# Optimization experiments

Hardware: AMD Instinct MI355X
Metric: run time of the kernel (lower is better)

The kernel has to match this reference:

```python
import jax, jax.numpy as jnp
import numpy as np

B, N, C = 8, 4096, 768
H = 12
D = C // H  # 64


def setup_inputs() -> dict:
    key = jax.random.key(0)
    k1, k2, k3 = jax.random.split(key, 3)
    x = jax.random.normal(k1, (B, N, C), dtype=jnp.float32)
    Wqkv = jax.random.normal(k2, (C, 3 * C), dtype=jnp.float32) * (C ** -0.5)
    Wproj = jax.random.normal(k3, (C, C), dtype=jnp.float32) * (C ** -0.5)
    bproj = jnp.zeros((C,), dtype=jnp.float32)
    return {"x": x, "Wqkv": Wqkv, "Wproj": Wproj, "bproj": bproj}


def reference(x, Wqkv, Wproj, bproj):
    b, n, c = x.shape
    qkv = x @ Wqkv  # [B,N,3C]
    qkv = qkv.reshape(b, n, 3, H, D).transpose(2, 0, 3, 1, 4)  # [3,B,H,N,D]
    q, k, v = qkv[0], qkv[1], qkv[2]
    # softmax over the sequence axis (dim=-2 in torch => N)
    k = jax.nn.softmax(k, axis=-2)
    # context: [B,H,D,D] -- small d x d intermediate
    context = jnp.einsum('bhnd,bhne->bhde', k, v)
    out = jnp.einsum('bhnd,bhde->bhne', q, context)  # [B,H,N,D]
    out = out.transpose(0, 2, 1, 3).reshape(b, n, c)  # b h n d -> b n (h d)
    return out @ Wproj + bproj
```

## Files before the change

kernel.cpp:

```cpp
#include <hip/hip_runtime.h>
#include <cstdint>
#include <cstddef>


typedef __bf16 bf8_t __attribute__((ext_vector_type(8)));
typedef float f4_t __attribute__((ext_vector_type(4)));

#define DEV_INLINE __device__ __forceinline__

DEV_INLINE void gload16(const void* g, void* l) {
  __builtin_amdgcn_global_load_lds(
      (const __attribute__((address_space(1))) void*)g,
      (__attribute__((address_space(3))) void*)l, 16, 0, 0);
}

__global__ __launch_bounds__(256) void cast_f32_bf16(const float* __restrict__ in,
                                                     __bf16* __restrict__ out, int n4) {
  int i = blockIdx.x * 256 + threadIdx.x;
  if (i >= n4) return;
  float4 f = ((const float4*)in)[i];
  union { __bf16 h[4]; uint2 u; } o;
  o.h[0] = (__bf16)f.x; o.h[1] = (__bf16)f.y; o.h[2] = (__bf16)f.z; o.h[3] = (__bf16)f.w;
  ((uint2*)out)[i] = o.u;
}

__global__ __launch_bounds__(256) void transpose_cast(const float* __restrict__ in,
                                                      __bf16* __restrict__ out, int R, int C) {
  __shared__ float t[64][65];
  const int tilesR = R >> 6;
  const int tr = blockIdx.x % tilesR, tc = blockIdx.x / tilesR;
  const int tx = threadIdx.x & 63, ty = threadIdx.x >> 6;
  const int r0 = tr * 64, c0 = tc * 64;
#pragma unroll
  for (int p = 0; p < 16; p++) {
    int r = p * 4 + ty;
    t[r][tx] = in[(size_t)(r0 + r) * C + c0 + tx];
  }
  __syncthreads();
#pragma unroll
  for (int p = 0; p < 16; p++) {
    int c = p * 4 + ty;
    out[(size_t)(c0 + c) * R + r0 + tx] = (__bf16)t[tx][c];
  }
}

__global__ __launch_bounds__(256) void wq_cast(const float* __restrict__ in,
                                               __bf16* __restrict__ out) {
  int o = blockIdx.x * 256 + threadIdx.x;
  int r = o / 768, c = o - r * 768;
  out[o] = (__bf16)in[r * 2304 + c];
}


#define SA_(buf, u, kc) gload16(gA + (size_t)((u) * 64) * 768 + (kc), dAl + (buf) * 16384 + (u) * 4096)
#define SB_(buf, u, kc) gload16(gB + (size_t)((u) * 64) * 768 + (kc), dBl + (buf) * 8192 + (u) * 4096)

#define PH_(q, STAGE, TAIL) do {                                              \
    bf8_t af[2][2], bfr[2][2];                                                \
    _Pragma("unroll") for (int i_ = 0; i_ < 2; i_++)                          \
      _Pragma("unroll") for (int ks_ = 0; ks_ < 2; ks_++) {                   \
        af[i_][ks_]  = *(const bf8_t*)(aB + offA[2 * ((q) >> 1) + i_][ks_]);  \
        bfr[i_][ks_] = *(const bf8_t*)(bB + offB[2 * ((q) & 1) + i_][ks_]);   \
      }                                                                       \
    STAGE;                                                                    \
    __builtin_amdgcn_s_barrier();                                             \
    __builtin_amdgcn_s_setprio(1);                                            \
    _Pragma("unroll") for (int ks_ = 0; ks_ < 2; ks_++)                       \
      _Pragma("unroll") for (int i_ = 0; i_ < 2; i_++)                        \
        _Pragma("unroll") for (int j_ = 0; j_ < 2; j_++)                      \
          acc[2 * ((q) >> 1) + i_][2 * ((q) & 1) + j_] =                      \
            __builtin_amdgcn_mfma_f32_16x16x32_bf16(af[i_][ks_], bfr[j_][ks_],\
              acc[2 * ((q) >> 1) + i_][2 * ((q) & 1) + j_], 0, 0, 0);         \
    __builtin_amdgcn_s_setprio(0);                                            \
    TAIL;                                                                     \
    __builtin_amdgcn_s_barrier();                                             \
  } while (0)

#define MAIN_LOOP() do {                                                      \
    SA_(0, 0, 0); SA_(0, 1, 0); SA_(0, 2, 0); SA_(0, 3, 0);                   \
    SB_(0, 0, 0); SB_(0, 1, 0);                                               \
    SA_(1, 0, 64); SA_(1, 1, 64); SA_(1, 2, 64); SA_(1, 3, 64);               \
    SB_(1, 0, 64); SB_(1, 1, 64);                                             \
    asm volatile("s_waitcnt vmcnt(6)" ::: "memory");                          \
    __builtin_amdgcn_s_barrier();                                             \
    int cur = 0;                                                              \
    for (int t = 0; t < 10; t++) {                                            \
      const __bf16* aB = sA + cur * 16384;                                    \
      const __bf16* bB = sB + cur * 8192;                                     \
      int nx = cur + 2; if (nx > 2) nx -= 3;                                  \
      const int kc = (t + 2) * 64;                                            \
      PH_(0, { SA_(nx, 0, kc); SA_(nx, 1, kc); }, {});                        \
      PH_(1, { SA_(nx, 2, kc); SA_(nx, 3, kc); }, {});                        \
      PH_(2, { SB_(nx, 0, kc); }, {});                                        \
      PH_(3, { SB_(nx, 1, kc); },                                             \
          { asm volatile("s_waitcnt vmcnt(6)" ::: "memory"); });              \
      cur++; if (cur > 2) cur = 0;                                            \
    }                                                                         \
    { const __bf16* aB = sA + cur * 16384;                                    \
      const __bf16* bB = sB + cur * 8192;                                     \
      PH_(0, {}, {}); PH_(1, {}, {}); PH_(2, {}, {});                         \
      PH_(3, {}, { asm volatile("s_waitcnt vmcnt(0)" ::: "memory"); });       \
      cur++; if (cur > 2) cur = 0; }                                          \
    { const __bf16* aB = sA + cur * 16384;                                    \
      const __bf16* bB = sB + cur * 8192;                                     \
      PH_(0, {}, {}); PH_(1, {}, {}); PH_(2, {}, {}); PH_(3, {}, {}); }       \
  } while (0)

#define GEMM_SETUP()                                                          \
  const int tid = threadIdx.x;                                                \
  const int trow = tid >> 3;                                                  \
  const int gcol = ((tid & 7) ^ (trow & 7)) * 8;                              \
  __bf16* dAl = sA + tid * 8;                                                 \
  __bf16* dBl = sB + tid * 8;                                                 \
  const int lane = tid & 63, wv = tid >> 6;                                   \
  const int wm = wv >> 1, wn = wv & 1;                                        \
  const int lr = lane & 15, quad = lane >> 4, rsw = lr & 7;                   \
  int offA[4][2], offB[4][2];                                                 \
  _Pragma("unroll") for (int f_ = 0; f_ < 4; f_++)                            \
    _Pragma("unroll") for (int ks_ = 0; ks_ < 2; ks_++) {                     \
      offA[f_][ks_] = (wm * 64 + f_ * 16 + lr) * 64 + (((ks_ * 4 + quad) ^ rsw) * 8); \
      offB[f_][ks_] = (wn * 64 + f_ * 16 + lr) * 64 + (((ks_ * 4 + quad) ^ rsw) * 8); \
    }                                                                         \
  f4_t acc[4][4];                                                             \
  _Pragma("unroll") for (int i_ = 0; i_ < 4; i_++)                            \
    _Pragma("unroll") for (int j_ = 0; j_ < 4; j_++)                          \
      acc[i_][j_] = (f4_t){0.f, 0.f, 0.f, 0.f};

__global__ __launch_bounds__(512, 2) void gemm1_kv(const __bf16* __restrict__ A,
                                                   const __bf16* __restrict__ B,
                                                   __bf16* __restrict__ KTo,
                                                   __bf16* __restrict__ VTo) {
  __shared__ __bf16 sA[3 * 16384];
  __shared__ __bf16 sB[3 * 8192];
  const int xcd = blockIdx.x & 7, g = blockIdx.x >> 3;
  const int mt = xcd * 16 + g / 12, nt = g % 12;
  GEMM_SETUP();
  const __bf16* gA = A + (size_t)(mt * 256 + trow) * 768 + gcol;
  const __bf16* gB = B + (size_t)(nt * 128 + trow) * 768 + gcol;

  MAIN_LOOP();

  const int s = nt / 6;
  __bf16* T = s ? VTo : KTo;
  const int colbase = (nt % 6) * 128 + wn * 64;
  const int bidx = mt >> 4;
  const int nbase = (mt & 15) * 256 + wm * 64 + quad * 4;
#pragma unroll
  for (int ci = 0; ci < 4; ci++) {
    int col = colbase + ci * 16 + lr;
    int h = col >> 6, d = col & 63;
    __bf16* Tp = T + ((size_t)(bidx * 12 + h) * 64 + d) * 4096;
#pragma unroll
    for (int ri = 0; ri < 4; ri++) {
      union { __bf16 h4[4]; uint2 u2; } pk;
#pragma unroll
      for (int r = 0; r < 4; r++) pk.h4[r] = (__bf16)acc[ri][ci][r];
      *(uint2*)&Tp[nbase + ri * 16] = pk.u2;
    }
  }
}

__global__ __launch_bounds__(256) void stats_rows(const __bf16* __restrict__ KT,
                                                  float2* __restrict__ stats) {
  __shared__ float red[8];
  const __bf16* p = KT + (size_t)blockIdx.x * 4096;
  const int tid = threadIdx.x, lane = tid & 63, wv = tid >> 6;
  bf8_t x0 = *(const bf8_t*)&p[tid * 16];
  bf8_t x1 = *(const bf8_t*)&p[tid * 16 + 8];
  float v[16];
#pragma unroll
  for (int k = 0; k < 8; k++) { v[k] = (float)x0[k]; v[8 + k] = (float)x1[k]; }
  float m = v[0];
#pragma unroll
  for (int k = 1; k < 16; k++) m = fmaxf(m, v[k]);
  for (int o = 32; o; o >>= 1) m = fmaxf(m, __shfl_xor(m, o, 64));
  if (lane == 0) red[wv] = m;
  __syncthreads();
  m = fmaxf(fmaxf(red[0], red[1]), fmaxf(red[2], red[3]));
  float s = 0.f;
#pragma unroll
  for (int k = 0; k < 16; k++) s += __expf(v[k] - m);
  for (int o = 32; o; o >>= 1) s += __shfl_xor(s, o, 64);
  if (lane == 0) red[4 + wv] = s;
  __syncthreads();
  if (tid == 0) {
    float st = red[4] + red[5] + red[6] + red[7];
    stats[blockIdx.x] = make_float2(m, 1.0f / st);
  }
}

__global__ __launch_bounds__(256) void ctx_kernel(const __bf16* __restrict__ KT,
                                                  const __bf16* __restrict__ VT,
                                                  const float2* __restrict__ stats,
                                                  float* __restrict__ part) {
  const int bh = blockIdx.x >> 3, kc = blockIdx.x & 7;
  const int tid = threadIdx.x, lane = tid & 63, wv = tid >> 6;
  const int wr = (wv >> 1) * 32, wc = (wv & 1) * 32;
  const int lr = lane & 15, quad = lane >> 4;
  const __bf16* Ab = KT + (size_t)bh * 64 * 4096;
  const __bf16* Bb = VT + (size_t)bh * 64 * 4096;
  float2 st[2];
  st[0] = stats[bh * 64 + wr + lr];
  st[1] = stats[bh * 64 + wr + 16 + lr];
  const f4_t fz = {0.f, 0.f, 0.f, 0.f};
  f4_t acc[2][2] = {{fz, fz}, {fz, fz}};
  const int kbeg = kc * 512;
  for (int k0 = kbeg; k0 < kbeg + 512; k0 += 32) {
    bf8_t a[2], b[2];
#pragma unroll
    for (int i = 0; i < 2; i++) {
      bf8_t raw = *(const bf8_t*)&Ab[(size_t)(wr + i * 16 + lr) * 4096 + k0 + quad * 8];
#pragma unroll
      for (int e = 0; e < 8; e++)
        a[i][e] = (__bf16)(__expf((float)raw[e] - st[i].x) * st[i].y);
    }
#pragma unroll
    for (int j = 0; j < 2; j++)
      b[j] = *(const bf8_t*)&Bb[(size_t)(wc + j * 16 + lr) * 4096 + k0 + quad * 8];
#pragma unroll
    for (int i = 0; i < 2; i++)
#pragma unroll
      for (int j = 0; j < 2; j++)
        acc[i][j] = __builtin_amdgcn_mfma_f32_16x16x32_bf16(a[i], b[j], acc[i][j], 0, 0, 0);
  }
  float* po = part + (size_t)blockIdx.x * 4096;
#pragma unroll
  for (int i = 0; i < 2; i++)
#pragma unroll
    for (int j = 0; j < 2; j++)
#pragma unroll
      for (int r = 0; r < 4; r++)
        po[(wr + i * 16 + quad * 4 + r) * 64 + wc + j * 16 + lr] = acc[i][j][r];
}

__global__ __launch_bounds__(256) void wfused_kernel(const float* __restrict__ part,
                                                     const __bf16* __restrict__ WpT,
                                                     __bf16* __restrict__ B2T) {
  __shared__ __bf16 sctx[64 * 64];
  const int bh = blockIdx.x, cblk = blockIdx.y;
  const int b = bh / 12, h = bh % 12;
  const int tid = threadIdx.x;
  for (int i = tid; i < 4096; i += 256) {
    float s = 0.f;
#pragma unroll
    for (int kc = 0; kc < 8; kc++) s += part[(size_t)(bh * 8 + kc) * 4096 + i];
    sctx[i] = (__bf16)s;
  }
  __syncthreads();
  const int lane = tid & 63, wv = tid >> 6, lr = lane & 15, quad = lane >> 4;
  const int c0 = cblk * 192 + wv * 48;
  const f4_t fz = {0.f, 0.f, 0.f, 0.f};
  f4_t acc[3][4];
#pragma unroll
  for (int i = 0; i < 3; i++)
#pragma unroll
    for (int j = 0; j < 4; j++) acc[i][j] = fz;
#pragma unroll
  for (int k0 = 0; k0 < 64; k0 += 32) {
    bf8_t a[3], bq[4];
#pragma unroll
    for (int i = 0; i < 3; i++)
      a[i] = *(const bf8_t*)&WpT[(size_t)(c0 + i * 16 + lr) * 768 + h * 64 + k0 + quad * 8];
#pragma unroll
    for (int j = 0; j < 4; j++)
      bq[j] = *(const bf8_t*)&sctx[(j * 16 + lr) * 64 + k0 + quad * 8];
#pragma unroll
    for (int i = 0; i < 3; i++)
#pragma unroll
      for (int j = 0; j < 4; j++)
        acc[i][j] = __builtin_amdgcn_mfma_f32_16x16x32_bf16(a[i], bq[j], acc[i][j], 0, 0, 0);
  }
#pragma unroll
  for (int i = 0; i < 3; i++)
#pragma unroll
    for (int j = 0; j < 4; j++)
#pragma unroll
      for (int r = 0; r < 4; r++) {
        int c = c0 + i * 16 + quad * 4 + r;
        int d = j * 16 + lr;
        B2T[((size_t)b * 768 + c) * 768 + h * 64 + d] = (__bf16)acc[i][j][r];
      }
}

__global__ __launch_bounds__(256) void combine_kernel(const __bf16* __restrict__ B2Tall,
                                                      const __bf16* __restrict__ Wq,
                                                      __bf16* __restrict__ Wcomb) {
  constexpr int LD = 768, BK = 32, KTOT = 768;
  __shared__ __bf16 sAc[64 * 32];
  __shared__ __bf16 sBc[64 * 32];
  const int b = blockIdx.x / 144, rem = blockIdx.x % 144;
  const int mt = rem / 12, nt = rem % 12;
  const __bf16* A = B2Tall + (size_t)b * 768 * 768;
  const int tid = threadIdx.x, lane = tid & 63, wv = tid >> 6;
  const int wr = (wv >> 1) * 32, wc = (wv & 1) * 32;
  const int lr = lane & 15, quad = lane >> 4;

  const int e0 = tid * 8;
  const int srow = e0 >> 5, skk = e0 & 31;
  const __bf16* gA = A + (size_t)(mt * 64 + srow) * LD + skk;
  const __bf16* gB = Wq + (size_t)(nt * 64 + srow) * LD + skk;

  const f4_t fz = {0.f, 0.f, 0.f, 0.f};
  f4_t acc[2][2] = {{fz, fz}, {fz, fz}};

  for (int k0 = 0; k0 < KTOT; k0 += BK) {
    gload16(gA, &sAc[e0]);
    gload16(gB, &sBc[e0]);
    gA += BK; gB += BK;
    __syncthreads();
    bf8_t a[2], bq[2];
#pragma unroll
    for (int i = 0; i < 2; i++)
      a[i] = *(const bf8_t*)&sAc[(wr + i * 16 + lr) * 32 + quad * 8];
#pragma unroll
    for (int j = 0; j < 2; j++)
      bq[j] = *(const bf8_t*)&sBc[(wc + j * 16 + lr) * 32 + quad * 8];
#pragma unroll
    for (int i = 0; i < 2; i++)
#pragma unroll
      for (int j = 0; j < 2; j++)
        acc[i][j] = __builtin_amdgcn_mfma_f32_16x16x32_bf16(a[i], bq[j], acc[i][j], 0, 0, 0);
    __syncthreads();
  }
  __bf16* C = Wcomb + (size_t)b * 768 * 768;
  const int row0 = mt * 64 + wr, col0 = nt * 64 + wc;
#pragma unroll
  for (int i = 0; i < 2; i++)
#pragma unroll
    for (int j = 0; j < 2; j++)
#pragma unroll
      for (int r = 0; r < 4; r++)
        C[(size_t)(row0 + i * 16 + quad * 4 + r) * 768 + col0 + j * 16 + lr] =
            (__bf16)acc[i][j][r];
}

__global__ __launch_bounds__(512, 2) void gemm2_out(const __bf16* __restrict__ A,
                                                    const __bf16* __restrict__ Ball,
                                                    float* __restrict__ C,
                                                    const float* __restrict__ bias) {
  __shared__ __bf16 sA[3 * 16384];
  __shared__ __bf16 sB[3 * 8192];
  const int xcd = blockIdx.x & 7, g = blockIdx.x >> 3;
  const int mt = xcd * 16 + g / 6, nt = g % 6;
  const __bf16* B = Ball + (size_t)(mt >> 4) * 768 * 768;
  GEMM_SETUP();
  const __bf16* gA = A + (size_t)(mt * 256 + trow) * 768 + gcol;
  const __bf16* gB = B + (size_t)(nt * 128 + trow) * 768 + gcol;

  MAIN_LOOP();

  const int row0 = mt * 256 + wm * 64 + quad * 4;
  const int col0 = nt * 128 + wn * 64;
#pragma unroll
  for (int ci = 0; ci < 4; ci++) {
    int col = col0 + ci * 16 + lr;
    float bv = bias[col];
#pragma unroll
    for (int ri = 0; ri < 4; ri++) {
#pragma unroll
      for (int r = 0; r < 4; r++)
        C[(size_t)(row0 + ri * 16 + r) * 768 + col] = acc[ri][ci][r] + bv;
    }
  }
}

extern "C" void kernel_launch(void* const* d_in, const int* in_sizes, int n_in,
                              void* d_out, int out_size, void* d_ws, size_t ws_size,
                              hipStream_t stream) {
  const float* x = (const float*)d_in[0];
  const float* Wqkv = (const float*)d_in[1];
  const float* Wproj = (const float*)d_in[2];
  const float* bproj = (const float*)d_in[3];
  float* out = (float*)d_out;

  char* ws = (char*)d_ws;
  __bf16* Xb    = (__bf16*)(ws + 0);
  __bf16* KT    = (__bf16*)(ws + 50331648);
  __bf16* VT    = (__bf16*)(ws + 100663296);
  __bf16* WqkvT = (__bf16*)(ws + 150994944);
  float2* stats = (float2*)(ws + 150994944);
  __bf16* Wqc   = (__bf16*)(ws + 154533888);
  __bf16* WpT   = (__bf16*)(ws + 155713536);
  float*  part  = (float*)(ws + 156893184);
  __bf16* B2T   = (__bf16*)(ws + 169476096);
  __bf16* Wcomb = (__bf16*)(ws + 178913280);

  cast_f32_bf16<<<24576, 256, 0, stream>>>(x, Xb, 25165824 / 4);
  transpose_cast<<<12 * 36, 256, 0, stream>>>(Wqkv, WqkvT, 768, 2304);
  wq_cast<<<(768 * 768) / 256, 256, 0, stream>>>(Wqkv, Wqc);
  transpose_cast<<<12 * 12, 256, 0, stream>>>(Wproj, WpT, 768, 768);
  gemm1_kv<<<1536, 512, 0, stream>>>(Xb, WqkvT + 768 * 768, KT, VT);
  stats_rows<<<6144, 256, 0, stream>>>(KT, stats);
  ctx_kernel<<<96 * 8, 256, 0, stream>>>(KT, VT, stats, part);
  wfused_kernel<<<dim3(96, 4), 256, 0, stream>>>(part, WpT, B2T);
  combine_kernel<<<1152, 256, 0, stream>>>(B2T, Wqc, Wcomb);
  gemm2_out<<<768, 512, 0, stream>>>(Xb, Wcomb, out, bproj);
}
```

Baseline: 438.6 us.

## Enlarge GEMM tiles to 256x256 with BK=32 and 8x4 accumulators per wave

```diff
diff --git a/kernel.cpp b/kernel.cpp
--- a/kernel.cpp
+++ b/kernel.cpp
@@ -52,110 +52,121 @@
 }
 
 
-#define SA_(buf, u, kc) gload16(gA + (size_t)((u) * 64) * 768 + (kc), dAl + (buf) * 16384 + (u) * 4096)
-#define SB_(buf, u, kc) gload16(gB + (size_t)((u) * 64) * 768 + (kc), dBl + (buf) * 8192 + (u) * 4096)
-
-#define PH_(q, STAGE, TAIL) do {                                              \
-    bf8_t af[2][2], bfr[2][2];                                                \
-    _Pragma("unroll") for (int i_ = 0; i_ < 2; i_++)                          \
-      _Pragma("unroll") for (int ks_ = 0; ks_ < 2; ks_++) {                   \
-        af[i_][ks_]  = *(const bf8_t*)(aB + offA[2 * ((q) >> 1) + i_][ks_]);  \
-        bfr[i_][ks_] = *(const bf8_t*)(bB + offB[2 * ((q) & 1) + i_][ks_]);   \
-      }                                                                       \
-    STAGE;                                                                    \
+#define MFMA16(aa, bb, cc) cc = __builtin_amdgcn_mfma_f32_16x16x32_bf16(aa, bb, cc, 0, 0, 0)
+
+#define SAu(buf, u, kc) gload16(gA + (size_t)((u) * 128) * 768 + (kc),        \
+                                sA + (buf) * 8192 + (u) * 4096 + tid * 8)
+#define SBu(buf, u, kc) gload16(gB + (size_t)((u) * 128) * 768 + (kc),        \
+                                sB + (buf) * 8192 + (u) * 4096 + tid * 8)
+#define STAGE_T(buf, kc) do { SAu(buf,0,kc); SAu(buf,1,kc); SBu(buf,0,kc); SBu(buf,1,kc); } while (0)
+
+#define G_SETUP()                                                             \
+  const int tid = threadIdx.x;                                                \
+  const int srow = tid >> 2;                                                  \
+  const int gcol = ((tid & 3) ^ (srow & 3)) * 8;                              \
+  const int lane = tid & 63, wv = tid >> 6;                                   \
+  const int wm = wv >> 2, wn = wv & 3;                                        \
+  const int lr = lane & 15, quad = lane >> 4;                                 \
+  const int ksw = (quad ^ (lr & 3)) * 8;                                      \
+  const int offA0 = (wm * 128 + lr) * 32 + ksw;                               \
+  const int offB0 = (wn * 64 + lr) * 32 + ksw;                                \
+  f4_t acc[8][4];                                                             \
+  _Pragma("unroll") for (int i_ = 0; i_ < 8; i_++)                            \
+    _Pragma("unroll") for (int j_ = 0; j_ < 4; j_++)                          \
+      acc[i_][j_] = (f4_t){0.f, 0.f, 0.f, 0.f};
+
+#define G_ITER(SA_STAGE, SB_STAGE, TAILV) do {                                \
+    const __bf16* aBp = sA + cur * 8192;                                      \
+    const __bf16* bBp = sB + cur * 8192;                                      \
+    bf8_t a0, a1, a2, a3, b0, b1, b2, b3;                                     \
+    a0 = *(const bf8_t*)(aBp + offA0);                                        \
+    a1 = *(const bf8_t*)(aBp + offA0 + 512);                                  \
+    a2 = *(const bf8_t*)(aBp + offA0 + 1024);                                 \
+    a3 = *(const bf8_t*)(aBp + offA0 + 1536);                                 \
+    b0 = *(const bf8_t*)(bBp + offB0);                                        \
+    b1 = *(const bf8_t*)(bBp + offB0 + 512);                                  \
+    b2 = *(const bf8_t*)(bBp + offB0 + 1024);                                 \
+    b3 = *(const bf8_t*)(bBp + offB0 + 1536);                                 \
+    SA_STAGE;                                                                 \
     __builtin_amdgcn_s_barrier();                                             \
     __builtin_amdgcn_s_setprio(1);                                            \
-    _Pragma("unroll") for (int ks_ = 0; ks_ < 2; ks_++)                       \
-      _Pragma("unroll") for (int i_ = 0; i_ < 2; i_++)                        \
-        _Pragma("unroll") for (int j_ = 0; j_ < 2; j_++)                      \
-          acc[2 * ((q) >> 1) + i_][2 * ((q) & 1) + j_] =                      \
-            __builtin_amdgcn_mfma_f32_16x16x32_bf16(af[i_][ks_], bfr[j_][ks_],\
-              acc[2 * ((q) >> 1) + i_][2 * ((q) & 1) + j_], 0, 0, 0);         \
+    MFMA16(a0, b0, acc[0][0]); MFMA16(a0, b1, acc[0][1]);                     \
+    MFMA16(a0, b2, acc[0][2]); MFMA16(a0, b3, acc[0][3]);                     \
+    MFMA16(a1, b0, acc[1][0]); MFMA16(a1, b1, acc[1][1]);                     \
+    MFMA16(a1, b2, acc[1][2]); MFMA16(a1, b3, acc[1][3]);                     \
+    MFMA16(a2, b0, acc[2][0]); MFMA16(a2, b1, acc[2][1]);                     \
+    MFMA16(a2, b2, acc[2][2]); MFMA16(a2, b3, acc[2][3]);                     \
+    MFMA16(a3, b0, acc[3][0]); MFMA16(a3, b1, acc[3][1]);                     \
+    MFMA16(a3, b2, acc[3][2]); MFMA16(a3, b3, acc[3][3]);                     \
     __builtin_amdgcn_s_setprio(0);                                            \
-    TAIL;                                                                     \
+    __builtin_amdgcn_s_barrier();                                             \
+    a0 = *(const bf8_t*)(aBp + offA0 + 2048);                                 \
+    a1 = *(const bf8_t*)(aBp + offA0 + 2560);                                 \
+    a2 = *(const bf8_t*)(aBp + offA0 + 3072);                                 \
+    a3 = *(const bf8_t*)(aBp + offA0 + 3584);                                 \
+    SB_STAGE;                                                                 \
+    __builtin_amdgcn_s_barrier();                                             \
+    __builtin_amdgcn_s_setprio(1);                                            \
+    MFMA16(a0, b0, acc[4][0]); MFMA16(a0, b1, acc[4][1]);                     \
+    MFMA16(a0, b2, acc[4][2]); MFMA16(a0, b3, acc[4][3]);                     \
+    MFMA16(a1, b0, acc[5][0]); MFMA16(a1, b1, acc[5][1]);                     \
+    MFMA16(a1, b2, acc[5][2]); MFMA16(a1, b3, acc[5][3]);                     \
+    MFMA16(a2, b0, acc[6][0]); MFMA16(a2, b1, acc[6][1]);                     \
+    MFMA16(a2, b2, acc[6][2]); MFMA16(a2, b3, acc[6][3]);                     \
+    MFMA16(a3, b0, acc[7][0]); MFMA16(a3, b1, acc[7][1]);                     \
+    MFMA16(a3, b2, acc[7][2]); MFMA16(a3, b3, acc[7][3]);                     \
+    __builtin_amdgcn_s_setprio(0);                                            \
+    TAILV;                                                                    \
     __builtin_amdgcn_s_barrier();                                             \
   } while (0)
 
-#define MAIN_LOOP() do {                                                      \
-    SA_(0, 0, 0); SA_(0, 1, 0); SA_(0, 2, 0); SA_(0, 3, 0);                   \
-    SB_(0, 0, 0); SB_(0, 1, 0);                                               \
-    SA_(1, 0, 64); SA_(1, 1, 64); SA_(1, 2, 64); SA_(1, 3, 64);               \
-    SB_(1, 0, 64); SB_(1, 1, 64);                                             \
-    asm volatile("s_waitcnt vmcnt(6)" ::: "memory");                          \
+#define G_MAIN() do {                                                         \
+    STAGE_T(0, 0); STAGE_T(1, 32);                                            \
+    asm volatile("s_waitcnt vmcnt(4)" ::: "memory");                          \
     __builtin_amdgcn_s_barrier();                                             \
     int cur = 0;                                                              \
-    for (int t = 0; t < 10; t++) {                                            \
-      const __bf16* aB = sA + cur * 16384;                                    \
-      const __bf16* bB = sB + cur * 8192;                                     \
+    for (int t = 0; t < 22; t++) {                                            \
       int nx = cur + 2; if (nx > 2) nx -= 3;                                  \
-      const int kc = (t + 2) * 64;                                            \
-      PH_(0, { SA_(nx, 0, kc); SA_(nx, 1, kc); }, {});                        \
-      PH_(1, { SA_(nx, 2, kc); SA_(nx, 3, kc); }, {});                        \
-      PH_(2, { SB_(nx, 0, kc); }, {});                                        \
-      PH_(3, { SB_(nx, 1, kc); },                                             \
-          { asm volatile("s_waitcnt vmcnt(6)" ::: "memory"); });              \
+      const int kc = t * 32 + 64;                                             \
+      G_ITER({ SAu(nx, 0, kc); SAu(nx, 1, kc); },                             \
+             { SBu(nx, 0, kc); SBu(nx, 1, kc); },                             \
+             { asm volatile("s_waitcnt vmcnt(4)" ::: "memory"); });           \
       cur++; if (cur > 2) cur = 0;                                            \
     }                                                                         \
-    { const __bf16* aB = sA + cur * 16384;                                    \
-      const __bf16* bB = sB + cur * 8192;                                     \
-      PH_(0, {}, {}); PH_(1, {}, {}); PH_(2, {}, {});                         \
-      PH_(3, {}, { asm volatile("s_waitcnt vmcnt(0)" ::: "memory"); });       \
-      cur++; if (cur > 2) cur = 0; }                                          \
-    { const __bf16* aB = sA + cur * 16384;                                    \
-      const __bf16* bB = sB + cur * 8192;                                     \
-      PH_(0, {}, {}); PH_(1, {}, {}); PH_(2, {}, {}); PH_(3, {}, {}); }       \
+    G_ITER({}, {}, { asm volatile("s_waitcnt vmcnt(0)" ::: "memory"); });     \
+    cur++; if (cur > 2) cur = 0;                                              \
+    G_ITER({}, {}, {});                                                       \
   } while (0)
-
-#define GEMM_SETUP()                                                          \
-  const int tid = threadIdx.x;                                                \
-  const int trow = tid >> 3;                                                  \
-  const int gcol = ((tid & 7) ^ (trow & 7)) * 8;                              \
-  __bf16* dAl = sA + tid * 8;                                                 \
-  __bf16* dBl = sB + tid * 8;                                                 \
-  const int lane = tid & 63, wv = tid >> 6;                                   \
-  const int wm = wv >> 1, wn = wv & 1;                                        \
-  const int lr = lane & 15, quad = lane >> 4, rsw = lr & 7;                   \
-  int offA[4][2], offB[4][2];                                                 \
-  _Pragma("unroll") for (int f_ = 0; f_ < 4; f_++)                            \
-    _Pragma("unroll") for (int ks_ = 0; ks_ < 2; ks_++) {                     \
-      offA[f_][ks_] = (wm * 64 + f_ * 16 + lr) * 64 + (((ks_ * 4 + quad) ^ rsw) * 8); \
-      offB[f_][ks_] = (wn * 64 + f_ * 16 + lr) * 64 + (((ks_ * 4 + quad) ^ rsw) * 8); \
-    }                                                                         \
-  f4_t acc[4][4];                                                             \
-  _Pragma("unroll") for (int i_ = 0; i_ < 4; i_++)                            \
-    _Pragma("unroll") for (int j_ = 0; j_ < 4; j_++)                          \
-      acc[i_][j_] = (f4_t){0.f, 0.f, 0.f, 0.f};
 
 __global__ __launch_bounds__(512, 2) void gemm1_kv(const __bf16* __restrict__ A,
                                                    const __bf16* __restrict__ B,
                                                    __bf16* __restrict__ KTo,
                                                    __bf16* __restrict__ VTo) {
-  __shared__ __bf16 sA[3 * 16384];
+  __shared__ __bf16 sA[3 * 8192];
   __shared__ __bf16 sB[3 * 8192];
   const int xcd = blockIdx.x & 7, g = blockIdx.x >> 3;
-  const int mt = xcd * 16 + g / 12, nt = g % 12;
-  GEMM_SETUP();
-  const __bf16* gA = A + (size_t)(mt * 256 + trow) * 768 + gcol;
-  const __bf16* gB = B + (size_t)(nt * 128 + trow) * 768 + gcol;
-
-  MAIN_LOOP();
-
-  const int s = nt / 6;
-  __bf16* T = s ? VTo : KTo;
-  const int colbase = (nt % 6) * 128 + wn * 64;
-  const int bidx = mt >> 4;
-  const int nbase = (mt & 15) * 256 + wm * 64 + quad * 4;
+  const int mt = xcd * 16 + g / 6, nt = g % 6;
+  G_SETUP();
+  const __bf16* gA = A + (size_t)(mt * 256 + srow) * 768 + gcol;
+  const __bf16* gB = B + (size_t)(nt * 256 + srow) * 768 + gcol;
+
+  G_MAIN();
+
+  const int sKV = (nt >= 3);
+  __bf16* T = sKV ? VTo : KTo;
+  const int cw = (nt - sKV * 3) * 256 + wn * 64;
+  const int b = mt >> 4;
+  const int n0 = (mt & 15) * 256 + wm * 128 + quad * 4;
 #pragma unroll
   for (int ci = 0; ci < 4; ci++) {
-    int col = colbase + ci * 16 + lr;
-    int h = col >> 6, d = col & 63;
-    __bf16* Tp = T + ((size_t)(bidx * 12 + h) * 64 + d) * 4096;
-#pragma unroll
-    for (int ri = 0; ri < 4; ri++) {
+    int cc = cw + ci * 16;
+    __bf16* Tp = T + ((size_t)(b * 12 + (cc >> 6)) * 64 + (cc & 63) + lr) * 4096;
+#pragma unroll
+    for (int ri = 0; ri < 8; ri++) {
       union { __bf16 h4[4]; uint2 u2; } pk;
 #pragma unroll
       for (int r = 0; r < 4; r++) pk.h4[r] = (__bf16)acc[ri][ci][r];
-      *(uint2*)&Tp[nbase + ri * 16] = pk.u2;
+      *(uint2*)&Tp[n0 + ri * 16] = pk.u2;
     }
   }
 }
@@ -338,25 +349,25 @@
                                                     const __bf16* __restrict__ Ball,
                                                     float* __restrict__ C,
                                                     const float* __restrict__ bias) {
-  __shared__ __bf16 sA[3 * 16384];
+  __shared__ __bf16 sA[3 * 8192];
   __shared__ __bf16 sB[3 * 8192];
   const int xcd = blockIdx.x & 7, g = blockIdx.x >> 3;
-  const int mt = xcd * 16 + g / 6, nt = g % 6;
+  const int mt = xcd * 16 + g / 3, nt = g % 3;
   const __bf16* B = Ball + (size_t)(mt >> 4) * 768 * 768;
-  GEMM_SETUP();
-  const __bf16* gA = A + (size_t)(mt * 256 + trow) * 768 + gcol;
-  const __bf16* gB = B + (size_t)(nt * 128 + trow) * 768 + gcol;
-
-  MAIN_LOOP();
-
-  const int row0 = mt * 256 + wm * 64 + quad * 4;
-  const int col0 = nt * 128 + wn * 64;
+  G_SETUP();
+  const __bf16* gA = A + (size_t)(mt * 256 + srow) * 768 + gcol;
+  const __bf16* gB = B + (size_t)(nt * 256 + srow) * 768 + gcol;
+
+  G_MAIN();
+
+  const int row0 = mt * 256 + wm * 128 + quad * 4;
+  const int col0 = nt * 256 + wn * 64;
 #pragma unroll
   for (int ci = 0; ci < 4; ci++) {
     int col = col0 + ci * 16 + lr;
     float bv = bias[col];
 #pragma unroll
-    for (int ri = 0; ri < 4; ri++) {
+    for (int ri = 0; ri < 8; ri++) {
 #pragma unroll
       for (int r = 0; r < 4; r++)
         C[(size_t)(row0 + ri * 16 + r) * 768 + col] = acc[ri][ci][r] + bv;
@@ -389,10 +400,10 @@
   transpose_cast<<<12 * 36, 256, 0, stream>>>(Wqkv, WqkvT, 768, 2304);
   wq_cast<<<(768 * 768) / 256, 256, 0, stream>>>(Wqkv, Wqc);
   transpose_cast<<<12 * 12, 256, 0, stream>>>(Wproj, WpT, 768, 768);
-  gemm1_kv<<<1536, 512, 0, stream>>>(Xb, WqkvT + 768 * 768, KT, VT);
+  gemm1_kv<<<768, 512, 0, stream>>>(Xb, WqkvT + 768 * 768, KT, VT);
   stats_rows<<<6144, 256, 0, stream>>>(KT, stats);
   ctx_kernel<<<96 * 8, 256, 0, stream>>>(KT, VT, stats, part);
   wfused_kernel<<<dim3(96, 4), 256, 0, stream>>>(part, WpT, B2T);
   combine_kernel<<<1152, 256, 0, stream>>>(B2T, Wqc, Wcomb);
-  gemm2_out<<<768, 512, 0, stream>>>(Xb, Wcomb, out, bproj);
-}
+  gemm2_out<<<384, 512, 0, stream>>>(Xb, Wcomb, out, bproj);
+}
```

New measurement: 428.5 us. 2.3% less time.
